# Kernel tuning notes

Measured on AMD Instinct MI355X. Metric: run time of the kernel, lower is better.

## Reference

```python
import jax, jax.numpy as jnp
import numpy as np

NUM_NODES = 100000
D_IN = 64
D_OUT = 64
NUM_EDGES = 1200000


def setup_inputs() -> dict:
    key = jax.random.key(0)
    k1, k2, k3, k4 = jax.random.split(key, 4)
    features = jax.random.normal(k1, (NUM_NODES, D_IN), dtype=jnp.float32)
    edge_index = jax.random.randint(k2, (2, NUM_EDGES), 0, NUM_NODES, dtype=jnp.int64)
    # Linear(input_dim*2 -> output_dim) parameters
    W = jax.random.normal(k3, (2 * D_IN, D_OUT), dtype=jnp.float32) / np.sqrt(2 * D_IN)
    b = jax.random.normal(k4, (D_OUT,), dtype=jnp.float32) * 0.01
    return {"features": features, "edge_index": edge_index, "W": W, "b": b}


def reference(features, edge_index, W, b):
    num_nodes = features.shape[0]
    src, dst = edge_index[0], edge_index[1]
    # gather source-node features for every edge: [E, D]
    src_feats = features[src]
    # segment-sum into destination nodes (mean aggregation)
    neigh_sum = jax.ops.segment_sum(src_feats, dst, num_segments=num_nodes)
    degree = jax.ops.segment_sum(jnp.ones_like(dst, dtype=features.dtype), dst,
                                 num_segments=num_nodes)
    degree = jnp.clip(degree, 1.0)
    neigh_mean = neigh_sum / degree[:, None]
    # concat self + neighbor features, then linear (dropout = identity in eval)
    combined = jnp.concatenate([features, neigh_mean], axis=-1)
    return combined @ W + b
```

## Files before the change

### kernel.cpp

```cpp
#include <hip/hip_runtime.h>

#define N_NODES 100000
#define D 64
#define N_EDGES 1200000
#define NCB 391
#define NBLK 256
#define PAD 16
#define CHUNK ((N_EDGES + NBLK - 1) / NBLK)

typedef __attribute__((ext_vector_type(8))) short short8v;
typedef __attribute__((ext_vector_type(8))) unsigned short ushort8v;
typedef __attribute__((ext_vector_type(4))) float f32x4;

__device__ __forceinline__ unsigned short f2bf(float x) {
    unsigned int b = __float_as_uint(x);
    b += 0x7FFFu + ((b >> 16) & 1u);
    return (unsigned short)(b >> 16);
}
__device__ __forceinline__ float bf2f(unsigned short u) {
    return __uint_as_float((unsigned int)u << 16);
}

__global__ __launch_bounds__(256) void bin_hist(
    const int* __restrict__ eidx, int* __restrict__ hist, int* __restrict__ totP,
    const float* __restrict__ feat, ushort* __restrict__ fb,
    const float* __restrict__ W, ushort* __restrict__ wb)
{
    __shared__ int h[NCB];
    for (int i = threadIdx.x; i < NCB; i += 256) h[i] = 0;
    __syncthreads();
    const int blk = blockIdx.x;

    if (blk < 32) {
        int g  = blk * 256 + threadIdx.x;
        int j  = g & 7;
        int l  = (g >> 3) & 63;
        int c4 = (g >> 9) & 3;
        int tt = g >> 11;
        int k   = 32 * tt + ((l >> 4) << 3) + j;
        int col = 16 * c4 + (l & 15);
        wb[g] = f2bf(W[k * 64 + col]);
    }

    const int beg = blk * CHUNK;
    const int end = min(beg + CHUNK, N_EDGES);
    for (int e = beg + threadIdx.x; e < end; e += 256)
        atomicAdd(&h[eidx[N_EDGES + e] >> 8], 1);

    const int total4 = N_NODES * D / 4;
    for (int i = blk * 256 + threadIdx.x; i < total4; i += NBLK * 256) {
        float4 v = ((const float4*)feat)[i];
        ushort4 o;
        o.x = f2bf(v.x); o.y = f2bf(v.y); o.z = f2bf(v.z); o.w = f2bf(v.w);
        ((ushort4*)fb)[i] = o;
    }

    __syncthreads();
    for (int i = threadIdx.x; i < NCB; i += 256) {
        int v = h[i];
        hist[blk * NCB + i] = v;
        if (v) atomicAdd(&totP[i * PAD], v);
    }
}

__global__ __launch_bounds__(256) void rstart(
    const int* __restrict__ totP, const int* __restrict__ hist,
    int* __restrict__ boff, int* __restrict__ runstart, int* __restrict__ offs)
{
    __shared__ int red[256];
    __shared__ int pfx[256];
    __shared__ int bo_s;

    const int tid = threadIdx.x;
    const int i   = blockIdx.x;

    int p = 0;
    for (int j = tid; j < i; j += 256) p += totP[j * PAD];
    red[tid] = p;
    __syncthreads();
    for (int off = 128; off > 0; off >>= 1) {
        if (tid < off) red[tid] += red[tid + off];
        __syncthreads();
    }
    if (tid == 0) {
        bo_s = red[0];
        boff[i] = red[0];
        if (i == 0) { boff[NCB] = N_EDGES; offs[N_NODES] = N_EDGES; }
    }
    __syncthreads();

    int v = hist[tid * NCB + i];
    pfx[tid] = v;
    __syncthreads();
    for (int off = 1; off < 256; off <<= 1) {
        int x = (tid >= off) ? pfx[tid - off] : 0;
        __syncthreads();
        pfx[tid] += x;
        __syncthreads();
    }
    runstart[tid * NCB + i] = bo_s + pfx[tid] - v;
}

__global__ __launch_bounds__(256) void bin_fill(
    const int* __restrict__ eidx, const int* __restrict__ runstart,
    unsigned int* __restrict__ pairs)
{
    __shared__ int lcur[NCB];
    const int blk = blockIdx.x;
    for (int i = threadIdx.x; i < NCB; i += 256) lcur[i] = runstart[blk * NCB + i];
    __syncthreads();
    const int beg = blk * CHUNK;
    const int end = min(beg + CHUNK, N_EDGES);
    for (int e = beg + threadIdx.x; e < end; e += 256) {
        int src = eidx[e];
        int dst = eidx[N_EDGES + e];
        int pos = atomicAdd(&lcur[dst >> 8], 1);
        pairs[pos] = ((unsigned int)src << 8) | (unsigned int)(dst & 255);
    }
}

__global__ __launch_bounds__(256) void fine_sort(
    const unsigned int* __restrict__ pairs,
    const int* __restrict__ boff,
    int* __restrict__ offs,
    int* __restrict__ csr)
{
    __shared__ int cnt[256];
    __shared__ int pfx[256];
    __shared__ int lcur[256];

    const int tid = threadIdx.x;
    const int b   = blockIdx.x;
    const int beg = boff[b];
    const int end = boff[b + 1];

    cnt[tid] = 0;
    __syncthreads();
    for (int j = beg + tid; j < end; j += 256)
        atomicAdd(&cnt[pairs[j] & 255], 1);
    __syncthreads();

    int v = cnt[tid];
    pfx[tid] = v;
    __syncthreads();
    for (int off = 1; off < 256; off <<= 1) {
        int x = (tid >= off) ? pfx[tid - off] : 0;
        __syncthreads();
        pfx[tid] += x;
        __syncthreads();
    }
    int ex = pfx[tid] - v;
    lcur[tid] = ex;
    int gn = b * 256 + tid;
    if (gn < N_NODES) offs[gn] = beg + ex;
    __syncthreads();

    for (int j = beg + tid; j < end; j += 256) {
        unsigned int p = pairs[j];
        int pos = beg + atomicAdd(&lcur[p & 255], 1);
        csr[pos] = (int)(p >> 8);
    }
}

#define MROW 72
#define S8(j) (((bf2f(v0[j])+bf2f(v1[j]))+(bf2f(v2[j])+bf2f(v3[j]))) \
             + ((bf2f(v4[j])+bf2f(v5[j]))+(bf2f(v6[j])+bf2f(v7[j]))))
#define S4(j) ((bf2f(v0[j])+bf2f(v1[j]))+(bf2f(v2[j])+bf2f(v3[j])))
__global__ __launch_bounds__(256) void agg_gemm(
    const ushort* __restrict__ fb,
    const int* __restrict__ offs,
    const int* __restrict__ csr,
    const ushort* __restrict__ wb,
    const float* __restrict__ bias,
    float* __restrict__ out)
{
    __shared__ __attribute__((aligned(16))) ushort wbl[8192];
    __shared__ __attribute__((aligned(16))) ushort means[32 * MROW];

    const int tid = threadIdx.x;
    const int n0  = blockIdx.x * 32;

    {
        const short8v* src = (const short8v*)wb;
        short8v* dst = (short8v*)wbl;
        #pragma unroll
        for (int r = 0; r < 4; ++r) dst[r * 256 + tid] = src[r * 256 + tid];
    }

    const int l    = tid & 7;
    const int node = tid >> 3;
    const int n    = n0 + node;

    const int beg = offs[n];
    const int end = offs[n + 1];
    const ushort8v* f8 = (const ushort8v*)fb;

    float s0=0.f,s1=0.f,s2=0.f,s3=0.f,s4=0.f,s5=0.f,s6=0.f,s7=0.f;
    int e = beg;
    for (; e + 8 <= end; e += 8) {
        int i0=csr[e+0], i1=csr[e+1], i2=csr[e+2], i3=csr[e+3];
        int i4=csr[e+4], i5=csr[e+5], i6=csr[e+6], i7=csr[e+7];
        ushort8v v0 = f8[(size_t)i0 * 8 + l];
        ushort8v v1 = f8[(size_t)i1 * 8 + l];
        ushort8v v2 = f8[(size_t)i2 * 8 + l];
        ushort8v v3 = f8[(size_t)i3 * 8 + l];
        ushort8v v4 = f8[(size_t)i4 * 8 + l];
        ushort8v v5 = f8[(size_t)i5 * 8 + l];
        ushort8v v6 = f8[(size_t)i6 * 8 + l];
        ushort8v v7 = f8[(size_t)i7 * 8 + l];
        s0 += S8(0); s1 += S8(1); s2 += S8(2); s3 += S8(3);
        s4 += S8(4); s5 += S8(5); s6 += S8(6); s7 += S8(7);
    }
    for (; e + 4 <= end; e += 4) {
        int i0=csr[e+0], i1=csr[e+1], i2=csr[e+2], i3=csr[e+3];
        ushort8v v0 = f8[(size_t)i0 * 8 + l];
        ushort8v v1 = f8[(size_t)i1 * 8 + l];
        ushort8v v2 = f8[(size_t)i2 * 8 + l];
        ushort8v v3 = f8[(size_t)i3 * 8 + l];
        s0 += S4(0); s1 += S4(1); s2 += S4(2); s3 += S4(3);
        s4 += S4(4); s5 += S4(5); s6 += S4(6); s7 += S4(7);
    }
    for (; e < end; ++e) {
        ushort8v v0 = f8[(size_t)csr[e] * 8 + l];
        s0 += bf2f(v0[0]); s1 += bf2f(v0[1]); s2 += bf2f(v0[2]); s3 += bf2f(v0[3]);
        s4 += bf2f(v0[4]); s5 += bf2f(v0[5]); s6 += bf2f(v0[6]); s7 += bf2f(v0[7]);
    }

    float dg = (float)(end - beg);
    dg = dg > 1.0f ? dg : 1.0f;
    float inv = 1.0f / dg;
    {
        ushort8v m;
        m[0]=f2bf(s0*inv); m[1]=f2bf(s1*inv); m[2]=f2bf(s2*inv); m[3]=f2bf(s3*inv);
        m[4]=f2bf(s4*inv); m[5]=f2bf(s5*inv); m[6]=f2bf(s6*inv); m[7]=f2bf(s7*inv);
        *(ushort8v*)(means + node * MROW + l * 8) = m;
    }
    __syncthreads();

    const int lane = tid & 63;
    const int wv   = tid >> 6;
    const int rt   = wv >> 1;
    const int cp   = wv & 1;
    const int kg   = lane >> 4;
    const int cl   = lane & 15;

    const ushort* frow = fb + (size_t)(n0 + rt * 16 + cl) * 64;
    const ushort* mrow = means + (rt * 16 + cl) * MROW;
    short8v a0 = *(const short8v*)(frow + kg * 8);
    short8v a1 = *(const short8v*)(frow + 32 + kg * 8);
    short8v a2 = *(const short8v*)(mrow + kg * 8);
    short8v a3 = *(const short8v*)(mrow + 32 + kg * 8);

    #pragma unroll
    for (int q = 0; q < 2; ++q) {
        const int c4 = cp * 2 + q;
        float bv = bias[c4 * 16 + cl];
        f32x4 acc = (f32x4){bv, bv, bv, bv};
        acc = __builtin_amdgcn_mfma_f32_16x16x32_bf16(
            a0, *(const short8v*)(wbl + (size_t)((0 * 4 + c4) * 64 + lane) * 8), acc, 0, 0, 0);
        acc = __builtin_amdgcn_mfma_f32_16x16x32_bf16(
            a1, *(const short8v*)(wbl + (size_t)((1 * 4 + c4) * 64 + lane) * 8), acc, 0, 0, 0);
        acc = __builtin_amdgcn_mfma_f32_16x16x32_bf16(
            a2, *(const short8v*)(wbl + (size_t)((2 * 4 + c4) * 64 + lane) * 8), acc, 0, 0, 0);
        acc = __builtin_amdgcn_mfma_f32_16x16x32_bf16(
            a3, *(const short8v*)(wbl + (size_t)((3 * 4 + c4) * 64 + lane) * 8), acc, 0, 0, 0);
        #pragma unroll
        for (int r = 0; r < 4; ++r)
            out[(size_t)(n0 + rt * 16 + kg * 4 + r) * 64 + c4 * 16 + cl] = acc[r];
    }
}

extern "C" void kernel_launch(void* const* d_in, const int* in_sizes, int n_in,
                              void* d_out, int out_size, void* d_ws, size_t ws_size,
                              hipStream_t stream) {
    const float* feat = (const float*)d_in[0];
    const int*   eidx = (const int*)d_in[1];
    const float* W    = (const float*)d_in[2];
    const float* bias = (const float*)d_in[3];
    float* out = (float*)d_out;

    int* hist     = (int*)d_ws;
    int* totP     = hist + NBLK * NCB;
    int* runstart = totP + NCB * PAD;
    int* boff     = runstart + NBLK * NCB;
    int* offs     = boff + NCB + 2;
    int* csr      = offs + N_NODES + 1;
    ushort* wb    = (ushort*)(csr + N_EDGES);
    unsigned int* pairs = (unsigned int*)(wb + 8192);
    ushort* fb    = (ushort*)(pairs + N_EDGES);

    hipMemsetAsync(totP, 0, (size_t)NCB * PAD * sizeof(int), stream);

    bin_hist<<<NBLK, 256, 0, stream>>>(eidx, hist, totP, feat, fb, W, wb);
    rstart<<<NCB, 256, 0, stream>>>(totP, hist, boff, runstart, offs);
    bin_fill<<<NBLK, 256, 0, stream>>>(eidx, runstart, pairs);
    fine_sort<<<NCB, 256, 0, stream>>>(pairs, boff, offs, csr);
    agg_gemm<<<N_NODES / 32, 256, 0, stream>>>(fb, offs, csr, wb, bias, out);
}
```

Before: 97.33 us.

## Balance neighbor aggregation across block edges with LDS atomic segment accumulation

Each block now splits the whole edge range of its 32 nodes evenly across 32 thread groups instead of one node per group, so skewed node degrees no longer leave groups idle. The CSR entries keep the packed destination low byte, so each group keeps running sums and flushes them to fp32 shared-memory accumulators with atomics whenever the destination changes. Mean scaling and bf16 conversion move into the MFMA operand load. The cost is extra branching per edge, LDS atomics and a larger shared buffer.

```diff
diff --git a/kernel.cpp b/kernel.cpp
--- a/kernel.cpp
+++ b/kernel.cpp
@@ -123,7 +123,7 @@
     const unsigned int* __restrict__ pairs,
     const int* __restrict__ boff,
     int* __restrict__ offs,
-    int* __restrict__ csr)
+    unsigned int* __restrict__ csr)
 {
     __shared__ int cnt[256];
     __shared__ int pfx[256];
@@ -158,24 +158,21 @@
     for (int j = beg + tid; j < end; j += 256) {
         unsigned int p = pairs[j];
         int pos = beg + atomicAdd(&lcur[p & 255], 1);
-        csr[pos] = (int)(p >> 8);
-    }
-}
-
-#define MROW 72
-#define S8(j) (((bf2f(v0[j])+bf2f(v1[j]))+(bf2f(v2[j])+bf2f(v3[j]))) \
-             + ((bf2f(v4[j])+bf2f(v5[j]))+(bf2f(v6[j])+bf2f(v7[j]))))
-#define S4(j) ((bf2f(v0[j])+bf2f(v1[j]))+(bf2f(v2[j])+bf2f(v3[j])))
+        csr[pos] = p;
+    }
+}
+
+#define MSTR 68
 __global__ __launch_bounds__(256) void agg_gemm(
     const ushort* __restrict__ fb,
     const int* __restrict__ offs,
-    const int* __restrict__ csr,
+    const unsigned int* __restrict__ csr,
     const ushort* __restrict__ wb,
     const float* __restrict__ bias,
     float* __restrict__ out)
 {
     __shared__ __attribute__((aligned(16))) ushort wbl[8192];
-    __shared__ __attribute__((aligned(16))) ushort means[32 * MROW];
+    __shared__ __attribute__((aligned(16))) float macc[32 * MSTR];
 
     const int tid = threadIdx.x;
     const int n0  = blockIdx.x * 32;
@@ -186,54 +183,61 @@
         #pragma unroll
         for (int r = 0; r < 4; ++r) dst[r * 256 + tid] = src[r * 256 + tid];
     }
-
-    const int l    = tid & 7;
-    const int node = tid >> 3;
-    const int n    = n0 + node;
-
-    const int beg = offs[n];
-    const int end = offs[n + 1];
+    #pragma unroll
+    for (int i = 0; i < 9; ++i) {
+        int idx = i * 256 + tid;
+        if (idx < 32 * MSTR) macc[idx] = 0.0f;
+    }
+    __syncthreads();
+
+    const int l = tid & 7;
+    const int o = tid >> 3;
+    const int base = offs[n0];
+    const int L    = offs[n0 + 32] - base;
+    const int ch   = (L + 31) >> 5;
+    const int lim  = base + L;
+    int j    = base + o * ch;
+    int jend = j + ch; if (jend > lim) jend = lim;
     const ushort8v* f8 = (const ushort8v*)fb;
-
-    float s0=0.f,s1=0.f,s2=0.f,s3=0.f,s4=0.f,s5=0.f,s6=0.f,s7=0.f;
-    int e = beg;
-    for (; e + 8 <= end; e += 8) {
-        int i0=csr[e+0], i1=csr[e+1], i2=csr[e+2], i3=csr[e+3];
-        int i4=csr[e+4], i5=csr[e+5], i6=csr[e+6], i7=csr[e+7];
-        ushort8v v0 = f8[(size_t)i0 * 8 + l];
-        ushort8v v1 = f8[(size_t)i1 * 8 + l];
-        ushort8v v2 = f8[(size_t)i2 * 8 + l];
-        ushort8v v3 = f8[(size_t)i3 * 8 + l];
-        ushort8v v4 = f8[(size_t)i4 * 8 + l];
-        ushort8v v5 = f8[(size_t)i5 * 8 + l];
-        ushort8v v6 = f8[(size_t)i6 * 8 + l];
-        ushort8v v7 = f8[(size_t)i7 * 8 + l];
-        s0 += S8(0); s1 += S8(1); s2 += S8(2); s3 += S8(3);
-        s4 += S8(4); s5 += S8(5); s6 += S8(6); s7 += S8(7);
-    }
-    for (; e + 4 <= end; e += 4) {
-        int i0=csr[e+0], i1=csr[e+1], i2=csr[e+2], i3=csr[e+3];
-        ushort8v v0 = f8[(size_t)i0 * 8 + l];
-        ushort8v v1 = f8[(size_t)i1 * 8 + l];
-        ushort8v v2 = f8[(size_t)i2 * 8 + l];
-        ushort8v v3 = f8[(size_t)i3 * 8 + l];
-        s0 += S4(0); s1 += S4(1); s2 += S4(2); s3 += S4(3);
-        s4 += S4(4); s5 += S4(5); s6 += S4(6); s7 += S4(7);
-    }
-    for (; e < end; ++e) {
-        ushort8v v0 = f8[(size_t)csr[e] * 8 + l];
-        s0 += bf2f(v0[0]); s1 += bf2f(v0[1]); s2 += bf2f(v0[2]); s3 += bf2f(v0[3]);
-        s4 += bf2f(v0[4]); s5 += bf2f(v0[5]); s6 += bf2f(v0[6]); s7 += bf2f(v0[7]);
-    }
-
-    float dg = (float)(end - beg);
-    dg = dg > 1.0f ? dg : 1.0f;
-    float inv = 1.0f / dg;
-    {
-        ushort8v m;
-        m[0]=f2bf(s0*inv); m[1]=f2bf(s1*inv); m[2]=f2bf(s2*inv); m[3]=f2bf(s3*inv);
-        m[4]=f2bf(s4*inv); m[5]=f2bf(s5*inv); m[6]=f2bf(s6*inv); m[7]=f2bf(s7*inv);
-        *(ushort8v*)(means + node * MROW + l * 8) = m;
+    const int nlow = n0 & 255;
+
+    float s[8];
+    #pragma unroll
+    for (int k = 0; k < 8; ++k) s[k] = 0.0f;
+    int cur = -1;
+
+    #define ACC1(P, V)                                                        \
+    {                                                                         \
+        int nd = (int)((P) & 255u) - nlow;                                    \
+        if (nd != cur) {                                                      \
+            if (cur >= 0) {                                                   \
+                float* mp = macc + cur * MSTR + l * 8;                        \
+                _Pragma("unroll")                                             \
+                for (int k = 0; k < 8; ++k) { atomicAdd(&mp[k], s[k]); s[k] = 0.0f; } \
+            }                                                                 \
+            cur = nd;                                                         \
+        }                                                                     \
+        _Pragma("unroll")                                                     \
+        for (int k = 0; k < 8; ++k) s[k] += bf2f((V)[k]);                     \
+    }
+
+    for (; j + 4 <= jend; j += 4) {
+        unsigned int p0 = csr[j], p1 = csr[j+1], p2 = csr[j+2], p3 = csr[j+3];
+        ushort8v v0 = f8[(size_t)(p0 >> 8) * 8 + l];
+        ushort8v v1 = f8[(size_t)(p1 >> 8) * 8 + l];
+        ushort8v v2 = f8[(size_t)(p2 >> 8) * 8 + l];
+        ushort8v v3 = f8[(size_t)(p3 >> 8) * 8 + l];
+        ACC1(p0, v0) ACC1(p1, v1) ACC1(p2, v2) ACC1(p3, v3)
+    }
+    for (; j < jend; ++j) {
+        unsigned int p = csr[j];
+        ushort8v v = f8[(size_t)(p >> 8) * 8 + l];
+        ACC1(p, v)
+    }
+    if (cur >= 0) {
+        float* mp = macc + cur * MSTR + l * 8;
+        #pragma unroll
+        for (int k = 0; k < 8; ++k) atomicAdd(&mp[k], s[k]);
     }
     __syncthreads();
 
@@ -244,12 +248,27 @@
     const int kg   = lane >> 4;
     const int cl   = lane & 15;
 
-    const ushort* frow = fb + (size_t)(n0 + rt * 16 + cl) * 64;
-    const ushort* mrow = means + (rt * 16 + cl) * MROW;
+    const int nn   = n0 + rt * 16 + cl;
+    const int deg  = offs[nn + 1] - offs[nn];
+    const float inv = 1.0f / (float)(deg > 1 ? deg : 1);
+
+    const ushort* frow = fb + (size_t)nn * 64;
     short8v a0 = *(const short8v*)(frow + kg * 8);
     short8v a1 = *(const short8v*)(frow + 32 + kg * 8);
-    short8v a2 = *(const short8v*)(mrow + kg * 8);
-    short8v a3 = *(const short8v*)(mrow + 32 + kg * 8);
+
+    const float* mrow = macc + (rt * 16 + cl) * MSTR;
+    f32x4 q0 = *(const f32x4*)(mrow + kg * 8);
+    f32x4 q1 = *(const f32x4*)(mrow + kg * 8 + 4);
+    f32x4 q2 = *(const f32x4*)(mrow + 32 + kg * 8);
+    f32x4 q3 = *(const f32x4*)(mrow + 32 + kg * 8 + 4);
+    short8v a2, a3;
+    #pragma unroll
+    for (int k = 0; k < 4; ++k) {
+        a2[k]     = (short)f2bf(q0[k] * inv);
+        a2[k + 4] = (short)f2bf(q1[k] * inv);
+        a3[k]     = (short)f2bf(q2[k] * inv);
+        a3[k + 4] = (short)f2bf(q3[k] * inv);
+    }
 
     #pragma unroll
     for (int q = 0; q < 2; ++q) {
@@ -284,7 +303,7 @@
     int* runstart = totP + NCB * PAD;
     int* boff     = runstart + NBLK * NCB;
     int* offs     = boff + NCB + 2;
-    int* csr      = offs + N_NODES + 1;
+    unsigned int* csr = (unsigned int*)(offs + N_NODES + 1);
     ushort* wb    = (ushort*)(csr + N_EDGES);
     unsigned int* pairs = (unsigned int*)(wb + 8192);
     ushort* fb    = (ushort*)(pairs + N_EDGES);
```

Measured after the change: 128.8 us. +32.4%, slower.

## Drop global bin-total atomics and memset; read weights directly from global in GEMM

Applied to the files above, without the earlier changes.

Removes the padded per-bin totals array, its memset, and the global atomicAdds in the histogram kernel. Each rstart block now computes its bin offset by summing the full per-block histogram directly. Separately, agg_gemm stops staging the 16KB bf16 weight matrix in shared memory and feeds MFMA B operands straight from global/L2. The aim is to save a memset launch, the atomics, and LDS use (which could raise occupancy), at the cost of far more redundant histogram reads in rstart (roughly 256×i loads per block) and uncached global weight loads per wave.

```diff
diff --git a/kernel.cpp b/kernel.cpp
--- a/kernel.cpp
+++ b/kernel.cpp
@@ -5,7 +5,6 @@
 #define N_EDGES 1200000
 #define NCB 391
 #define NBLK 256
-#define PAD 16
 #define CHUNK ((N_EDGES + NBLK - 1) / NBLK)
 
 typedef __attribute__((ext_vector_type(8))) short short8v;
@@ -22,7 +21,7 @@
 }
 
 __global__ __launch_bounds__(256) void bin_hist(
-    const int* __restrict__ eidx, int* __restrict__ hist, int* __restrict__ totP,
+    const int* __restrict__ eidx, int* __restrict__ hist,
     const float* __restrict__ feat, ushort* __restrict__ fb,
     const float* __restrict__ W, ushort* __restrict__ wb)
 {
@@ -56,15 +55,12 @@
     }
 
     __syncthreads();
-    for (int i = threadIdx.x; i < NCB; i += 256) {
-        int v = h[i];
-        hist[blk * NCB + i] = v;
-        if (v) atomicAdd(&totP[i * PAD], v);
-    }
+    for (int i = threadIdx.x; i < NCB; i += 256)
+        hist[blk * NCB + i] = h[i];
 }
 
 __global__ __launch_bounds__(256) void rstart(
-    const int* __restrict__ totP, const int* __restrict__ hist,
+    const int* __restrict__ hist,
     int* __restrict__ boff, int* __restrict__ runstart, int* __restrict__ offs)
 {
     __shared__ int red[256];
@@ -75,7 +71,9 @@
     const int i   = blockIdx.x;
 
     int p = 0;
-    for (int j = tid; j < i; j += 256) p += totP[j * PAD];
+    for (int blk = 0; blk < NBLK; ++blk)
+        for (int j = tid; j < i; j += 256)
+            p += hist[blk * NCB + j];
     red[tid] = p;
     __syncthreads();
     for (int off = 128; off > 0; off >>= 1) {
@@ -174,18 +172,10 @@
     const float* __restrict__ bias,
     float* __restrict__ out)
 {
-    __shared__ __attribute__((aligned(16))) ushort wbl[8192];
     __shared__ __attribute__((aligned(16))) ushort means[32 * MROW];
 
     const int tid = threadIdx.x;
     const int n0  = blockIdx.x * 32;
-
-    {
-        const short8v* src = (const short8v*)wb;
-        short8v* dst = (short8v*)wbl;
-        #pragma unroll
-        for (int r = 0; r < 4; ++r) dst[r * 256 + tid] = src[r * 256 + tid];
-    }
 
     const int l    = tid & 7;
     const int node = tid >> 3;
@@ -251,19 +241,21 @@
     short8v a2 = *(const short8v*)(mrow + kg * 8);
     short8v a3 = *(const short8v*)(mrow + 32 + kg * 8);
 
+    const short8v* wv8 = (const short8v*)wb;
+
     #pragma unroll
     for (int q = 0; q < 2; ++q) {
         const int c4 = cp * 2 + q;
         float bv = bias[c4 * 16 + cl];
         f32x4 acc = (f32x4){bv, bv, bv, bv};
         acc = __builtin_amdgcn_mfma_f32_16x16x32_bf16(
-            a0, *(const short8v*)(wbl + (size_t)((0 * 4 + c4) * 64 + lane) * 8), acc, 0, 0, 0);
-        acc = __builtin_amdgcn_mfma_f32_16x16x32_bf16(
-            a1, *(const short8v*)(wbl + (size_t)((1 * 4 + c4) * 64 + lane) * 8), acc, 0, 0, 0);
-        acc = __builtin_amdgcn_mfma_f32_16x16x32_bf16(
-            a2, *(const short8v*)(wbl + (size_t)((2 * 4 + c4) * 64 + lane) * 8), acc, 0, 0, 0);
-        acc = __builtin_amdgcn_mfma_f32_16x16x32_bf16(
-            a3, *(const short8v*)(wbl + (size_t)((3 * 4 + c4) * 64 + lane) * 8), acc, 0, 0, 0);
+            a0, wv8[(0 * 4 + c4) * 64 + lane], acc, 0, 0, 0);
+        acc = __builtin_amdgcn_mfma_f32_16x16x32_bf16(
+            a1, wv8[(1 * 4 + c4) * 64 + lane], acc, 0, 0, 0);
+        acc = __builtin_amdgcn_mfma_f32_16x16x32_bf16(
+            a2, wv8[(2 * 4 + c4) * 64 + lane], acc, 0, 0, 0);
+        acc = __builtin_amdgcn_mfma_f32_16x16x32_bf16(
+            a3, wv8[(3 * 4 + c4) * 64 + lane], acc, 0, 0, 0);
         #pragma unroll
         for (int r = 0; r < 4; ++r)
             out[(size_t)(n0 + rt * 16 + kg * 4 + r) * 64 + c4 * 16 + cl] = acc[r];
@@ -280,8 +272,7 @@
     float* out = (float*)d_out;
 
     int* hist     = (int*)d_ws;
-    int* totP     = hist + NBLK * NCB;
-    int* runstart = totP + NCB * PAD;
+    int* runstart = hist + NBLK * NCB;
     int* boff     = runstart + NBLK * NCB;
     int* offs     = boff + NCB + 2;
     int* csr      = offs + N_NODES + 1;
@@ -289,10 +280,8 @@
     unsigned int* pairs = (unsigned int*)(wb + 8192);
     ushort* fb    = (ushort*)(pairs + N_EDGES);
 
-    hipMemsetAsync(totP, 0, (size_t)NCB * PAD * sizeof(int), stream);
-
-    bin_hist<<<NBLK, 256, 0, stream>>>(eidx, hist, totP, feat, fb, W, wb);
-    rstart<<<NCB, 256, 0, stream>>>(totP, hist, boff, runstart, offs);
+    bin_hist<<<NBLK, 256, 0, stream>>>(eidx, hist, feat, fb, W, wb);
+    rstart<<<NCB, 256, 0, stream>>>(hist, boff, runstart, offs);
     bin_fill<<<NBLK, 256, 0, stream>>>(eidx, runstart, pairs);
     fine_sort<<<NCB, 256, 0, stream>>>(pairs, boff, offs, csr);
     agg_gemm<<<N_NODES / 32, 256, 0, stream>>>(fb, offs, csr, wb, bias, out);
```

New measurement: 190.6 us. 95.9% more time.
